# Performance work log

Hardware: AMD Instinct MI355X
Metric: run time of the kernel (lower is better)

Reference implementation:

```python
import jax, jax.numpy as jnp
import numpy as np

NEG = -9e15
EPS = 1e-5

def setup_inputs() -> dict:
    key = jax.random.key(0)
    k1, k2, k3, k4 = jax.random.split(key, 4)
    B, S, D = 4, 2048, 1024
    q = jax.random.normal(k1, (B, S, D), dtype=jnp.float32)
    k = jax.random.normal(k2, (B, S, D), dtype=jnp.float32)
    v = jax.random.normal(k3, (B, S, D), dtype=jnp.float32)
    mask = jax.random.randint(k4, (B, S, S), 0, 2, dtype=jnp.int32)
    gamma = jnp.ones((D,), dtype=jnp.float32)
    beta = jnp.zeros((D,), dtype=jnp.float32)
    return {"q": q, "k": k, "v": v, "mask": mask, "gamma": gamma, "beta": beta}

def reference(q, k, v, mask, gamma, beta):
    d_k = q.shape[-1]
    # scaled dot-product attention: [B,S,S] logits materialized as in original
    logits = jnp.einsum('bsd,btd->bst', q, k) / jnp.sqrt(jnp.asarray(d_k, q.dtype))
    logits = jnp.where(mask == 0, jnp.asarray(NEG, logits.dtype), logits)
    attn = jax.nn.softmax(logits, axis=-1)
    x = jnp.einsum('bst,btd->bsd', attn, v)
    # dropout is identity at inference; LayerNorm over last dim
    mu = jnp.mean(x, axis=-1, keepdims=True)
    var = jnp.mean(jnp.square(x - mu), axis=-1, keepdims=True)
    xhat = (x - mu) * jax.lax.rsqrt(var + EPS)
    return xhat * gamma + beta
```

## Files before the change

kernel.cpp:

```cpp
#include <hip/hip_runtime.h>
#include <hip/hip_bf16.h>

typedef unsigned short u16;
typedef unsigned long long u64;
typedef __attribute__((ext_vector_type(8))) short bf16x8;
typedef __attribute__((ext_vector_type(4))) float f32x4;
typedef __attribute__((ext_vector_type(4))) float float4v;
typedef __attribute__((ext_vector_type(4))) short short4v;
typedef __attribute__((ext_vector_type(4))) int int4v;

#define BB 4
#define SS 2048
#define DD 1024

__device__ __forceinline__ u16 f2bf(float x){
    unsigned u = __float_as_uint(x);
    return (u16)((u + 0x7fffu + ((u >> 16) & 1u)) >> 16);
}

#define GLD16(g, l) __builtin_amdgcn_global_load_lds( \
    (const __attribute__((address_space(1))) unsigned int*)(g), \
    (__attribute__((address_space(3))) unsigned int*)(l), 16, 0, 0)

#define SCHED0() __builtin_amdgcn_sched_barrier(0)
#define PH_PRE()  SCHED0(); __builtin_amdgcn_s_barrier(); SCHED0(); __builtin_amdgcn_s_setprio(1)
#define PH_POST() __builtin_amdgcn_s_setprio(0); SCHED0(); __builtin_amdgcn_s_barrier(); SCHED0()

__global__ __launch_bounds__(256) void prep_kernel(
    const float* __restrict__ q, const float* __restrict__ k,
    const float* __restrict__ v, const int* __restrict__ mask,
    u16* __restrict__ Qb, u16* __restrict__ Kb, u16* __restrict__ Vt,
    unsigned int* __restrict__ mbits, float* __restrict__ rowsum)
{
    const int bid = blockIdx.x;
    const int tid = threadIdx.x;

    if (bid < 4096){
        const float* in = (bid < 2048) ? q : k;
        u16* out = (bid < 2048) ? Qb : Kb;
        const float scale = (bid < 2048) ? 0.03125f : 1.0f;
        const int sb = bid & 2047;
#pragma unroll
        for (int kk = 0; kk < 4; ++kk){
            int i = sb * 1024 + kk * 256 + tid;
            float4v val = ((const float4v*)in)[i];
            short4v o;
            o[0] = (short)f2bf(val[0] * scale); o[1] = (short)f2bf(val[1] * scale);
            o[2] = (short)f2bf(val[2] * scale); o[3] = (short)f2bf(val[3] * scale);
            ((short4v*)out)[i] = o;
        }
    } else if (bid < 6144){
        __shared__ float tile[64][65];
        const int sb = bid - 4096;
        const int b  = sb >> 9;
        const int r  = sb & 511;
        const int s0 = (r >> 4) << 6;
        const int d0 = (r & 15) << 6;
        const int tx = tid & 15;
        const int ty = tid >> 4;
#pragma unroll
        for (int kk = 0; kk < 4; ++kk){
            const float* p = v + ((size_t)(b * SS + s0 + ty + 16 * kk) * DD) + d0 + tx * 4;
            float4v val = *(const float4v*)p;
            tile[ty + 16 * kk][tx * 4 + 0] = val[0];
            tile[ty + 16 * kk][tx * 4 + 1] = val[1];
            tile[ty + 16 * kk][tx * 4 + 2] = val[2];
            tile[ty + 16 * kk][tx * 4 + 3] = val[3];
        }
        __syncthreads();
#pragma unroll
        for (int kk = 0; kk < 4; ++kk){
            int dy = ty + 16 * kk;
            short4v o;
            o[0] = (short)f2bf(tile[tx * 4 + 0][dy]);
            o[1] = (short)f2bf(tile[tx * 4 + 1][dy]);
            o[2] = (short)f2bf(tile[tx * 4 + 2][dy]);
            o[3] = (short)f2bf(tile[tx * 4 + 3][dy]);
            *(short4v*)&Vt[((size_t)(b * DD + d0 + dy) * SS) + s0 + tx * 4] = o;
        }
    } else if (bid < 8192){
        const int i = (bid - 6144) * 256 + tid;
        const int4v* p = (const int4v*)mask + (size_t)i * 8;
        unsigned w = 0;
#pragma unroll
        for (int j = 0; j < 8; ++j){
            int4v vv = p[j];
            w |= (unsigned)(vv[0] != 0) << (j * 4 + 0);
            w |= (unsigned)(vv[1] != 0) << (j * 4 + 1);
            w |= (unsigned)(vv[2] != 0) << (j * 4 + 2);
            w |= (unsigned)(vv[3] != 0) << (j * 4 + 3);
        }
        mbits[i] = w;
    } else {
        rowsum[(bid - 8192) * 256 + tid] = 0.f;
    }
}

__global__ __launch_bounds__(512, 2) void qk_kernel(
    const u16* __restrict__ Qb, const u16* __restrict__ Kb,
    const u64* __restrict__ mbits, u16* __restrict__ P,
    float* __restrict__ rowsum)
{
    __shared__ __align__(16) u16 As[2][256 * 64];
    __shared__ __align__(16) u16 Bs[2][256 * 64];

    const int swz = ((blockIdx.x & 7) << 5) + (blockIdx.x >> 3);
    const int b   = swz >> 6;
    const int bx  = (swz >> 3) & 7;
    const int by  = swz & 7;
    const int row0 = bx << 8, col0 = by << 8;

    const int tid = threadIdx.x;
    const int wid = tid >> 6, lane = tid & 63;
    const int l16 = lane & 15, g4 = lane >> 4;
    const int wq = wid >> 2, wk = wid & 3;

    const int sr   = tid >> 3;
    const int scol = ((tid & 7) ^ (sr & 7)) << 3;
    const u16* gA = Kb + (size_t)(b * SS + col0 + sr) * DD + scol;
    const u16* gB = Qb + (size_t)(b * SS + row0 + sr) * DD + scol;
    char* const lA0 = (char*)As[0] + tid * 16;
    char* const lB0 = (char*)Bs[0] + tid * 16;
    char* const lA1 = (char*)As[1] + tid * 16;
    char* const lB1 = (char*)Bs[1] + tid * 16;

    const int kRow = (wk * 64  + l16) << 7;
    const int qRow = (wq * 128 + l16) << 7;
    const int cx0  = (g4 << 4) ^ ((l16 & 7) << 4);

    f32x4 acc[4][8];
    const f32x4 z4 = {0.f, 0.f, 0.f, 0.f};
#pragma unroll
    for (int i = 0; i < 4; ++i)
#pragma unroll
        for (int j = 0; j < 8; ++j) acc[i][j] = z4;

#define STAGE_QK(kt, la, lb) { \
    const u16* ga_ = gA + (kt) * 64; \
    const u16* gb_ = gB + (kt) * 64; \
    GLD16(ga_,            (la)); \
    GLD16(ga_ +  64 * DD, (la) + 8192); \
    GLD16(ga_ + 128 * DD, (la) + 16384); \
    GLD16(ga_ + 192 * DD, (la) + 24576); \
    GLD16(gb_,            (lb)); \
    GLD16(gb_ +  64 * DD, (lb) + 8192); \
    GLD16(gb_ + 128 * DD, (lb) + 16384); \
    GLD16(gb_ + 192 * DD, (lb) + 24576); }

#define LDQ8(Bb_, kx) { \
    const char* p_ = (const char*)(Bb_) + qRow + ((kx) ? (cx0 ^ 64) : cx0); \
    fq0 = *(const bf16x8*)(p_);          fq1 = *(const bf16x8*)(p_ + 2048); \
    fq2 = *(const bf16x8*)(p_ + 4096);   fq3 = *(const bf16x8*)(p_ + 6144); \
    fq4 = *(const bf16x8*)(p_ + 8192);   fq5 = *(const bf16x8*)(p_ + 10240); \
    fq6 = *(const bf16x8*)(p_ + 12288);  fq7 = *(const bf16x8*)(p_ + 14336); }

#define LDK2(Ab_, mh, kx) { \
    const char* p_ = (const char*)(Ab_) + kRow + (mh) * 4096 + ((kx) ? (cx0 ^ 64) : cx0); \
    fk0 = *(const bf16x8*)(p_); \
    fk1 = *(const bf16x8*)(p_ + 2048); }

#define MKROW(mi, fk) \
    acc[mi][0] = __builtin_amdgcn_mfma_f32_16x16x32_bf16(fk, fq0, acc[mi][0],0,0,0); \
    acc[mi][1] = __builtin_amdgcn_mfma_f32_16x16x32_bf16(fk, fq1, acc[mi][1],0,0,0); \
    acc[mi][2] = __builtin_amdgcn_mfma_f32_16x16x32_bf16(fk, fq2, acc[mi][2],0,0,0); \
    acc[mi][3] = __builtin_amdgcn_mfma_f32_16x16x32_bf16(fk, fq3, acc[mi][3],0,0,0); \
    acc[mi][4] = __builtin_amdgcn_mfma_f32_16x16x32_bf16(fk, fq4, acc[mi][4],0,0,0); \
    acc[mi][5] = __builtin_amdgcn_mfma_f32_16x16x32_bf16(fk, fq5, acc[mi][5],0,0,0); \
    acc[mi][6] = __builtin_amdgcn_mfma_f32_16x16x32_bf16(fk, fq6, acc[mi][6],0,0,0); \
    acc[mi][7] = __builtin_amdgcn_mfma_f32_16x16x32_bf16(fk, fq7, acc[mi][7],0,0,0);

    STAGE_QK(0, lA0, lB0);
    STAGE_QK(1, lA1, lB1);
    asm volatile("s_waitcnt vmcnt(8)" ::: "memory");
    SCHED0(); __builtin_amdgcn_s_barrier(); SCHED0();

#pragma unroll 1
    for (int it = 0; it < 8; ++it){
        bf16x8 fq0, fq1, fq2, fq3, fq4, fq5, fq6, fq7, fk0, fk1;
        LDK2(As[0], 0, 0); LDQ8(Bs[0], 0);
        PH_PRE(); MKROW(0,fk0) MKROW(1,fk1) PH_POST();
        LDK2(As[0], 1, 0);
        PH_PRE(); MKROW(2,fk0) MKROW(3,fk1) PH_POST();
        LDK2(As[0], 0, 1); LDQ8(Bs[0], 1);
        PH_PRE(); MKROW(0,fk0) MKROW(1,fk1) PH_POST();
        LDK2(As[0], 1, 1);
        PH_PRE(); MKROW(2,fk0) MKROW(3,fk1) PH_POST();
        if (it < 7){
            STAGE_QK(2*it+2, lA0, lB0);
            asm volatile("s_waitcnt vmcnt(8)" ::: "memory");
        } else {
            asm volatile("s_waitcnt vmcnt(0)" ::: "memory");
        }
        SCHED0(); __builtin_amdgcn_s_barrier(); SCHED0();
        LDK2(As[1], 0, 0); LDQ8(Bs[1], 0);
        PH_PRE(); MKROW(0,fk0) MKROW(1,fk1) PH_POST();
        LDK2(As[1], 1, 0);
        PH_PRE(); MKROW(2,fk0) MKROW(3,fk1) PH_POST();
        LDK2(As[1], 0, 1); LDQ8(Bs[1], 1);
        PH_PRE(); MKROW(0,fk0) MKROW(1,fk1) PH_POST();
        LDK2(As[1], 1, 1);
        PH_PRE(); MKROW(2,fk0) MKROW(3,fk1) PH_POST();
        if (it < 7){
            STAGE_QK(2*it+3, lA1, lB1);
            asm volatile("s_waitcnt vmcnt(8)" ::: "memory");
            SCHED0(); __builtin_amdgcn_s_barrier(); SCHED0();
        }
    }
#undef STAGE_QK
#undef LDQ8
#undef LDK2
#undef MKROW

#pragma unroll
    for (int nq = 0; nq < 8; ++nq){
        const int grow = row0 + wq * 128 + nq * 16 + l16;
        const size_t rbase = (size_t)(b * SS + grow) * SS;
        const u64 w64 = mbits[(size_t)(b * SS + grow) * 32 + by * 4 + wk];
        float rs = 0.f;
#pragma unroll
        for (int mk = 0; mk < 4; ++mk){
            const int bit0 = mk * 16 + g4 * 4;
            const int gcolb = col0 + wk * 64 + bit0;
            float e0 = ((w64 >> (bit0 + 0)) & 1ull) ? __expf(acc[mk][nq][0]) : 0.f;
            float e1 = ((w64 >> (bit0 + 1)) & 1ull) ? __expf(acc[mk][nq][1]) : 0.f;
            float e2 = ((w64 >> (bit0 + 2)) & 1ull) ? __expf(acc[mk][nq][2]) : 0.f;
            float e3 = ((w64 >> (bit0 + 3)) & 1ull) ? __expf(acc[mk][nq][3]) : 0.f;
            short4v pp;
            pp[0] = (short)f2bf(e0); pp[1] = (short)f2bf(e1);
            pp[2] = (short)f2bf(e2); pp[3] = (short)f2bf(e3);
            *(short4v*)&P[rbase + gcolb] = pp;
            rs += (e0 + e1) + (e2 + e3);
        }
        rs += __shfl_xor(rs, 16);
        rs += __shfl_xor(rs, 32);
        if (g4 == 0) atomicAdd(&rowsum[b * SS + grow], rs);
    }
}

__global__ __launch_bounds__(512, 2) void pv_kernel(
    const u16* __restrict__ P, const u16* __restrict__ Vt,
    const float* __restrict__ rowsum, u16* __restrict__ Xn)
{
    __shared__ __align__(16) u16 As[2][128 * 64];
    __shared__ __align__(16) u16 Bs[2][256 * 64];

    const int swz = ((blockIdx.x & 7) << 5) + (blockIdx.x >> 3);
    const int b   = swz >> 6;
    const int bx  = (swz >> 2) & 15;
    const int by  = swz & 3;
    const int row0 = bx << 7, col0 = by << 8;

    const int tid = threadIdx.x;
    const int wid = tid >> 6, lane = tid & 63;
    const int l16 = lane & 15, g4 = lane >> 4;
    const int wr = wid >> 2, wc = wid & 3;

    const int sr   = tid >> 3;
    const int scol = ((tid & 7) ^ (sr & 7)) << 3;
    const u16* gA = P  + (size_t)(b * SS + row0 + sr) * SS + scol;
    const u16* gB = Vt + (size_t)(b * DD + col0 + sr) * SS + scol;
    char* const lA0 = (char*)As[0] + tid * 16;
    char* const lB0 = (char*)Bs[0] + tid * 16;
    char* const lA1 = (char*)As[1] + tid * 16;
    char* const lB1 = (char*)Bs[1] + tid * 16;

    const int aRow = (wr * 64 + l16) << 7;
    const int bRow = (wc * 64 + l16) << 7;
    const int cx0  = (g4 << 4) ^ ((l16 & 7) << 4);

    f32x4 acc[4][4];
    const f32x4 z4 = {0.f, 0.f, 0.f, 0.f};
#pragma unroll
    for (int i = 0; i < 4; ++i)
#pragma unroll
        for (int j = 0; j < 4; ++j) acc[i][j] = z4;

#define STAGE_PV(kt, la, lb) { \
    const u16* ga_ = gA + (kt) * 64; \
    const u16* gb_ = gB + (kt) * 64; \
    GLD16(ga_,            (la)); \
    GLD16(ga_ +  64 * SS, (la) + 8192); \
    GLD16(gb_,            (lb)); \
    GLD16(gb_ +  64 * SS, (lb) + 8192); \
    GLD16(gb_ + 128 * SS, (lb) + 16384); \
    GLD16(gb_ + 192 * SS, (lb) + 24576); }

#define LDA2(Ab_, mh, kx) { \
    const char* p_ = (const char*)(Ab_) + aRow + (mh) * 4096 + ((kx) ? (cx0 ^ 64) : cx0); \
    fa0 = *(const bf16x8*)(p_); \
    fa1 = *(const bf16x8*)(p_ + 2048); }

#define LDB4(Bb_, kx) { \
    const char* p_ = (const char*)(Bb_) + bRow + ((kx) ? (cx0 ^ 64) : cx0); \
    fb0 = *(const bf16x8*)(p_); \
    fb1 = *(const bf16x8*)(p_ + 2048); \
    fb2 = *(const bf16x8*)(p_ + 4096); \
    fb3 = *(const bf16x8*)(p_ + 6144); }

#define MROWP(mi, fa) \
    acc[mi][0] = __builtin_amdgcn_mfma_f32_16x16x32_bf16(fa, fb0, acc[mi][0],0,0,0); \
    acc[mi][1] = __builtin_amdgcn_mfma_f32_16x16x32_bf16(fa, fb1, acc[mi][1],0,0,0); \
    acc[mi][2] = __builtin_amdgcn_mfma_f32_16x16x32_bf16(fa, fb2, acc[mi][2],0,0,0); \
    acc[mi][3] = __builtin_amdgcn_mfma_f32_16x16x32_bf16(fa, fb3, acc[mi][3],0,0,0);

    STAGE_PV(0, lA0, lB0);
    STAGE_PV(1, lA1, lB1);
    asm volatile("s_waitcnt vmcnt(6)" ::: "memory");
    SCHED0(); __builtin_amdgcn_s_barrier(); SCHED0();

#pragma unroll 1
    for (int it = 0; it < 16; ++it){
        bf16x8 fa0, fa1, fb0, fb1, fb2, fb3;
        LDA2(As[0], 0, 0); LDB4(Bs[0], 0);
        PH_PRE(); MROWP(0,fa0) MROWP(1,fa1) PH_POST();
        LDA2(As[0], 1, 0);
        PH_PRE(); MROWP(2,fa0) MROWP(3,fa1) PH_POST();
        LDA2(As[0], 0, 1); LDB4(Bs[0], 1);
        PH_PRE(); MROWP(0,fa0) MROWP(1,fa1) PH_POST();
        LDA2(As[0], 1, 1);
        PH_PRE(); MROWP(2,fa0) MROWP(3,fa1) PH_POST();
        if (it < 15){
            STAGE_PV(2*it+2, lA0, lB0);
            asm volatile("s_waitcnt vmcnt(6)" ::: "memory");
        } else {
            asm volatile("s_waitcnt vmcnt(0)" ::: "memory");
        }
        SCHED0(); __builtin_amdgcn_s_barrier(); SCHED0();
        LDA2(As[1], 0, 0); LDB4(Bs[1], 0);
        PH_PRE(); MROWP(0,fa0) MROWP(1,fa1) PH_POST();
        LDA2(As[1], 1, 0);
        PH_PRE(); MROWP(2,fa0) MROWP(3,fa1) PH_POST();
        LDA2(As[1], 0, 1); LDB4(Bs[1], 1);
        PH_PRE(); MROWP(0,fa0) MROWP(1,fa1) PH_POST();
        LDA2(As[1], 1, 1);
        PH_PRE(); MROWP(2,fa0) MROWP(3,fa1) PH_POST();
        if (it < 15){
            STAGE_PV(2*it+3, lA1, lB1);
            asm volatile("s_waitcnt vmcnt(6)" ::: "memory");
            SCHED0(); __builtin_amdgcn_s_barrier(); SCHED0();
        }
    }
#undef STAGE_PV
#undef LDA2
#undef LDB4
#undef MROWP

#pragma unroll
    for (int m = 0; m < 4; ++m){
        float inv[4];
#pragma unroll
        for (int r = 0; r < 4; ++r)
            inv[r] = 1.f / rowsum[b * SS + row0 + wr * 64 + m * 16 + g4 * 4 + r];
#pragma unroll
        for (int n = 0; n < 4; ++n){
            const int gcol = col0 + wc * 64 + n * 16 + l16;
#pragma unroll
            for (int r = 0; r < 4; ++r){
                const int grow = row0 + wr * 64 + m * 16 + g4 * 4 + r;
                Xn[(size_t)(b * SS + grow) * DD + gcol] = f2bf(acc[m][n][r] * inv[r]);
            }
        }
    }
}

__global__ __launch_bounds__(256) void ln_kernel(
    const u16* __restrict__ Xn, const float* __restrict__ gamma,
    const float* __restrict__ beta, float* __restrict__ out)
{
    __shared__ float red[2][4];
    const int row = blockIdx.x;
    const int t = threadIdx.x;
    short4v xv = *(const short4v*)&Xn[(size_t)row * DD + t * 4];
    float x[4];
#pragma unroll
    for (int j = 0; j < 4; ++j)
        x[j] = __uint_as_float(((unsigned)(u16)xv[j]) << 16);
    float s  = x[0] + x[1] + x[2] + x[3];
    float sq = x[0]*x[0] + x[1]*x[1] + x[2]*x[2] + x[3]*x[3];
#pragma unroll
    for (int d = 1; d < 64; d <<= 1){ s += __shfl_xor(s, d); sq += __shfl_xor(sq, d); }
    const int wv = t >> 6;
    if ((t & 63) == 0){ red[0][wv] = s; red[1][wv] = sq; }
    __syncthreads();
    float S  = red[0][0] + red[0][1] + red[0][2] + red[0][3];
    float Sq = red[1][0] + red[1][1] + red[1][2] + red[1][3];
    float mu = S * (1.f / 1024.f);
    float var = Sq * (1.f / 1024.f) - mu * mu;
    float rstd = rsqrtf(var + 1e-5f);
    float4v g  = *(const float4v*)&gamma[t * 4];
    float4v be = *(const float4v*)&beta[t * 4];
    float4v o;
#pragma unroll
    for (int j = 0; j < 4; ++j) o[j] = (x[j] - mu) * rstd * g[j] + be[j];
    *(float4v*)&out[(size_t)row * DD + t * 4] = o;
}

extern "C" void kernel_launch(void* const* d_in, const int* in_sizes, int n_in,
                              void* d_out, int out_size, void* d_ws, size_t ws_size,
                              hipStream_t stream) {
    const float* q     = (const float*)d_in[0];
    const float* k     = (const float*)d_in[1];
    const float* v     = (const float*)d_in[2];
    const int*   mask  = (const int*)d_in[3];
    const float* gamma = (const float*)d_in[4];
    const float* beta  = (const float*)d_in[5];
    float* out = (float*)d_out;

    u16* Qb = (u16*)d_ws;
    u16* Kb = Qb + (size_t)BB * SS * DD;
    u16* Vt = Kb + (size_t)BB * SS * DD;
    u16* P  = Vt + (size_t)BB * SS * DD;
    u16* Xn = P  + (size_t)BB * SS * SS;
    float* rowsum = (float*)(Xn + (size_t)BB * SS * DD);
    unsigned int* mbits = (unsigned int*)Xn;

    prep_kernel<<<8224, 256, 0, stream>>>(q, k, v, mask, Qb, Kb, Vt, mbits, rowsum);
    qk_kernel<<<256, 512, 0, stream>>>(Qb, Kb, (const u64*)mbits, P, rowsum);
    pv_kernel<<<256, 512, 0, stream>>>(P, Vt, rowsum, Xn);
    ln_kernel<<<BB * SS, 256, 0, stream>>>(Xn, gamma, beta, out);
}
```

Measured before the change: 139.5 us.

## Rework prep kernel with packed bf16 converts, wider stores and ballot mask bits

The prep kernel now converts to bf16 with the hardware v_cvt_pk_bf16_f32 instruction and writes 16-byte stores for Q/K and the transposed V. Mask packing moves from per-thread bit assembly over strided loads to coalesced loads plus wave ballots, which produces an interleaved bit layout. The qk kernel reads four u64 words per row and decodes that layout. The qk launch-bounds occupancy hint of 2 is also dropped. Together these aim to cut prep bandwidth and instruction overhead. The risks are LDS bank conflicts in the new transpose read pattern and a different register allocation in qk.

```diff
diff --git a/kernel.cpp b/kernel.cpp
--- a/kernel.cpp
+++ b/kernel.cpp
@@ -8,6 +8,8 @@
 typedef __attribute__((ext_vector_type(4))) float float4v;
 typedef __attribute__((ext_vector_type(4))) short short4v;
 typedef __attribute__((ext_vector_type(4))) int int4v;
+typedef __attribute__((ext_vector_type(4))) unsigned int u32x4;
+typedef __attribute__((ext_vector_type(4))) unsigned long long u64x4;
 
 #define BB 4
 #define SS 2048
@@ -16,6 +18,12 @@
 __device__ __forceinline__ u16 f2bf(float x){
     unsigned u = __float_as_uint(x);
     return (u16)((u + 0x7fffu + ((u >> 16) & 1u)) >> 16);
+}
+
+__device__ __forceinline__ unsigned cvtpk(float lo, float hi){
+    unsigned r;
+    asm("v_cvt_pk_bf16_f32 %0, %1, %2" : "=v"(r) : "v"(lo), "v"(hi));
+    return r;
 }
 
 #define GLD16(g, l) __builtin_amdgcn_global_load_lds( \
@@ -30,7 +38,7 @@
     const float* __restrict__ q, const float* __restrict__ k,
     const float* __restrict__ v, const int* __restrict__ mask,
     u16* __restrict__ Qb, u16* __restrict__ Kb, u16* __restrict__ Vt,
-    unsigned int* __restrict__ mbits, float* __restrict__ rowsum)
+    u64* __restrict__ mbits64, float* __restrict__ rowsum)
 {
     const int bid = blockIdx.x;
     const int tid = threadIdx.x;
@@ -41,13 +49,16 @@
         const float scale = (bid < 2048) ? 0.03125f : 1.0f;
         const int sb = bid & 2047;
 #pragma unroll
-        for (int kk = 0; kk < 4; ++kk){
-            int i = sb * 1024 + kk * 256 + tid;
-            float4v val = ((const float4v*)in)[i];
-            short4v o;
-            o[0] = (short)f2bf(val[0] * scale); o[1] = (short)f2bf(val[1] * scale);
-            o[2] = (short)f2bf(val[2] * scale); o[3] = (short)f2bf(val[3] * scale);
-            ((short4v*)out)[i] = o;
+        for (int u = 0; u < 2; ++u){
+            const int i8 = (sb * 256 + tid) * 2 + u;
+            float4v a = ((const float4v*)in)[i8 * 2];
+            float4v c = ((const float4v*)in)[i8 * 2 + 1];
+            u32x4 w;
+            w[0] = cvtpk(a[0] * scale, a[1] * scale);
+            w[1] = cvtpk(a[2] * scale, a[3] * scale);
+            w[2] = cvtpk(c[0] * scale, c[1] * scale);
+            w[3] = cvtpk(c[2] * scale, c[3] * scale);
+            ((u32x4*)out)[i8] = w;
         }
     } else if (bid < 6144){
         __shared__ float tile[64][65];
@@ -69,36 +80,43 @@
         }
         __syncthreads();
 #pragma unroll
-        for (int kk = 0; kk < 4; ++kk){
-            int dy = ty + 16 * kk;
-            short4v o;
-            o[0] = (short)f2bf(tile[tx * 4 + 0][dy]);
-            o[1] = (short)f2bf(tile[tx * 4 + 1][dy]);
-            o[2] = (short)f2bf(tile[tx * 4 + 2][dy]);
-            o[3] = (short)f2bf(tile[tx * 4 + 3][dy]);
-            *(short4v*)&Vt[((size_t)(b * DD + d0 + dy) * SS) + s0 + tx * 4] = o;
+        for (int u = 0; u < 2; ++u){
+            const int unit = u * 256 + tid;
+            const int d  = unit & 63;
+            const int sg = unit >> 6;
+            u32x4 w;
+            w[0] = cvtpk(tile[sg * 8 + 0][d], tile[sg * 8 + 1][d]);
+            w[1] = cvtpk(tile[sg * 8 + 2][d], tile[sg * 8 + 3][d]);
+            w[2] = cvtpk(tile[sg * 8 + 4][d], tile[sg * 8 + 5][d]);
+            w[3] = cvtpk(tile[sg * 8 + 6][d], tile[sg * 8 + 7][d]);
+            *(u32x4*)&Vt[((size_t)(b * DD + d0 + d) * SS) + s0 + sg * 8] = w;
         }
     } else if (bid < 8192){
-        const int i = (bid - 6144) * 256 + tid;
-        const int4v* p = (const int4v*)mask + (size_t)i * 8;
-        unsigned w = 0;
+        const int sb = bid - 6144;
+        const int tt = sb * 256 + tid;
+        const int lane = tid & 63;
 #pragma unroll
         for (int j = 0; j < 8; ++j){
-            int4v vv = p[j];
-            w |= (unsigned)(vv[0] != 0) << (j * 4 + 0);
-            w |= (unsigned)(vv[1] != 0) << (j * 4 + 1);
-            w |= (unsigned)(vv[2] != 0) << (j * 4 + 2);
-            w |= (unsigned)(vv[3] != 0) << (j * 4 + 3);
-        }
-        mbits[i] = w;
+            const int idx = j * 524288 + tt;
+            int4v mm = ((const int4v*)mask)[idx];
+            u64 b0 = __ballot(mm[0] != 0);
+            u64 b1 = __ballot(mm[1] != 0);
+            u64 b2 = __ballot(mm[2] != 0);
+            u64 b3 = __ballot(mm[3] != 0);
+            const int gw = idx >> 6;
+            if (lane < 4){
+                u64 w = (lane == 0) ? b0 : (lane == 1) ? b1 : (lane == 2) ? b2 : b3;
+                mbits64[(size_t)gw * 4 + lane] = w;
+            }
+        }
     } else {
         rowsum[(bid - 8192) * 256 + tid] = 0.f;
     }
 }
 
-__global__ __launch_bounds__(512, 2) void qk_kernel(
+__global__ __launch_bounds__(512) void qk_kernel(
     const u16* __restrict__ Qb, const u16* __restrict__ Kb,
-    const u64* __restrict__ mbits, u16* __restrict__ P,
+    const u64* __restrict__ mbits64, u16* __restrict__ P,
     float* __restrict__ rowsum)
 {
     __shared__ __align__(16) u16 As[2][256 * 64];
@@ -215,16 +233,16 @@
     for (int nq = 0; nq < 8; ++nq){
         const int grow = row0 + wq * 128 + nq * 16 + l16;
         const size_t rbase = (size_t)(b * SS + grow) * SS;
-        const u64 w64 = mbits[(size_t)(b * SS + grow) * 32 + by * 4 + wk];
+        u64x4 w = *(const u64x4*)&mbits64[((size_t)(b * SS + grow) * 8 + by) * 4];
         float rs = 0.f;
 #pragma unroll
         for (int mk = 0; mk < 4; ++mk){
-            const int bit0 = mk * 16 + g4 * 4;
-            const int gcolb = col0 + wk * 64 + bit0;
-            float e0 = ((w64 >> (bit0 + 0)) & 1ull) ? __expf(acc[mk][nq][0]) : 0.f;
-            float e1 = ((w64 >> (bit0 + 1)) & 1ull) ? __expf(acc[mk][nq][1]) : 0.f;
-            float e2 = ((w64 >> (bit0 + 2)) & 1ull) ? __expf(acc[mk][nq][2]) : 0.f;
-            float e3 = ((w64 >> (bit0 + 3)) & 1ull) ? __expf(acc[mk][nq][3]) : 0.f;
+            const int sh = wk * 16 + mk * 4 + g4;
+            const int gcolb = col0 + wk * 64 + mk * 16 + g4 * 4;
+            float e0 = ((w[0] >> sh) & 1ull) ? __expf(acc[mk][nq][0]) : 0.f;
+            float e1 = ((w[1] >> sh) & 1ull) ? __expf(acc[mk][nq][1]) : 0.f;
+            float e2 = ((w[2] >> sh) & 1ull) ? __expf(acc[mk][nq][2]) : 0.f;
+            float e3 = ((w[3] >> sh) & 1ull) ? __expf(acc[mk][nq][3]) : 0.f;
             short4v pp;
             pp[0] = (short)f2bf(e0); pp[1] = (short)f2bf(e1);
             pp[2] = (short)f2bf(e2); pp[3] = (short)f2bf(e3);
@@ -412,10 +430,10 @@
     u16* P  = Vt + (size_t)BB * SS * DD;
     u16* Xn = P  + (size_t)BB * SS * SS;
     float* rowsum = (float*)(Xn + (size_t)BB * SS * DD);
-    unsigned int* mbits = (unsigned int*)Xn;
-
-    prep_kernel<<<8224, 256, 0, stream>>>(q, k, v, mask, Qb, Kb, Vt, mbits, rowsum);
-    qk_kernel<<<256, 512, 0, stream>>>(Qb, Kb, (const u64*)mbits, P, rowsum);
+    u64* mbits64 = (u64*)Xn;
+
+    prep_kernel<<<8224, 256, 0, stream>>>(q, k, v, mask, Qb, Kb, Vt, mbits64, rowsum);
+    qk_kernel<<<256, 512, 0, stream>>>(Qb, Kb, mbits64, P, rowsum);
     pv_kernel<<<256, 512, 0, stream>>>(P, Vt, rowsum, Xn);
     ln_kernel<<<BB * SS, 256, 0, stream>>>(Xn, gamma, beta, out);
 }
```

Measured after the change: 142.2 us. About the same (+2.0%).
